# Optimization experiments

Measured on AMD Instinct MI355X. Metric: run time of the kernel, lower is better.

The kernel has to match this reference:

```python
import jax, jax.numpy as jnp
import numpy as np

N_HEAD = 16
HEAD_DIM = 32          # n_embed // n_head // 2
LAMBDA_INIT = 0.2      # 0.8 - 0.6*exp(-0.3*(layer-1)) with layer=1
ROPE_BASE = 10000.0
EPS = 1e-5


def _rope(x):
    # torchtune RotaryPositionalEmbeddings: interleaved adjacent pairs
    B, T, H, D = x.shape
    half = D // 2
    theta = ROPE_BASE ** (-(jnp.arange(half, dtype=jnp.float32) * 2.0 / D))  # [half]
    ang = jnp.arange(T, dtype=jnp.float32)[:, None] * theta[None, :]         # [T, half]
    cos = jnp.cos(ang)[None, :, None, :]
    sin = jnp.sin(ang)[None, :, None, :]
    xr = x.reshape(B, T, H, half, 2)
    x1, x2 = xr[..., 0], xr[..., 1]
    out = jnp.stack([x1 * cos - x2 * sin, x1 * sin + x2 * cos], axis=-1)
    return out.reshape(B, T, H, D).astype(x.dtype)


def reference(x, W_attn, W_proj, lambda_q1, lambda_k1, lambda_q2, lambda_k2):
    B, T, C = x.shape
    H, D = N_HEAD, HEAD_DIM
    qkv = x @ W_attn                              # [B,T,3C]
    q, k, v = jnp.split(qkv, 3, axis=-1)
    q = _rope(q.reshape(B, T, 2 * H, D)).transpose(0, 2, 1, 3)   # [B,2H,T,D]
    k = _rope(k.reshape(B, T, 2 * H, D)).transpose(0, 2, 1, 3)   # [B,2H,T,D]
    v = v.reshape(B, T, H, 2 * D).transpose(0, 2, 1, 3)          # [B,H,T,2D]

    lam = (jnp.exp(jnp.dot(lambda_q1, lambda_k1))
           - jnp.exp(jnp.dot(lambda_q2, lambda_k2)) + LAMBDA_INIT)

    # causal SDPA over both score paths (2H heads) in one pass, shared V
    scale = 1.0 / jnp.sqrt(jnp.asarray(D, x.dtype))
    scores = jnp.einsum('bhqd,bhkd->bhqk', q, k) * scale         # [B,2H,T,T]
    causal = jnp.tril(jnp.ones((T, T), dtype=bool))
    scores = jnp.where(causal, scores, jnp.finfo(scores.dtype).min)
    probs = jax.nn.softmax(scores, axis=-1)
    vv = jnp.concatenate([v, v], axis=1)                         # [B,2H,T,2D]
    A = jnp.einsum('bhqk,bhkd->bhqd', probs, vv)                 # [B,2H,T,2D]
    A1, A2 = A[:, :H], A[:, H:]

    diff = A1 - lam * A2                                         # [B,H,T,2D]
    # RMSNorm over last dim (2*head_dim), no affine, eps=1e-5
    diff = diff * jax.lax.rsqrt(jnp.mean(diff * diff, axis=-1, keepdims=True) + EPS)
    diff = (1.0 - LAMBDA_INIT) * diff
    out = diff.transpose(0, 2, 1, 3).reshape(B, T, C)
    return out @ W_proj


def setup_inputs() -> dict:
    key = jax.random.key(0)
    ks = jax.random.split(key, 7)
    B, T, C, D = 2, 2048, 1024, HEAD_DIM
    return {
        'x': jax.random.normal(ks[0], (B, T, C), jnp.float32),
        'W_attn': jax.random.normal(ks[1], (C, 3 * C), jnp.float32) * 0.02,
        'W_proj': jax.random.normal(ks[2], (C, C), jnp.float32) * 0.02,
        'lambda_q1': jax.random.normal(ks[3], (D,), jnp.float32) * 0.1,
        'lambda_k1': jax.random.normal(ks[4], (D,), jnp.float32) * 0.1,
        'lambda_q2': jax.random.normal(ks[5], (D,), jnp.float32) * 0.1,
        'lambda_k2': jax.random.normal(ks[6], (D,), jnp.float32) * 0.1,
    }
```

## Files before the change

### kernel.cpp

```cpp
#include <hip/hip_runtime.h>


typedef unsigned short u16;
typedef __bf16 bf16x8 __attribute__((ext_vector_type(8)));
typedef float f32x4 __attribute__((ext_vector_type(4)));
typedef float f32x16 __attribute__((ext_vector_type(16)));
typedef unsigned u32x2 __attribute__((ext_vector_type(2)));

__device__ __forceinline__ u16 f2bf(float f) {
  return __builtin_bit_cast(u16, (__bf16)f);
}
__device__ __forceinline__ float bf2f(u16 u) {
  return (float)__builtin_bit_cast(__bf16, u);
}
__device__ __forceinline__ unsigned pk2(float a, float b) {
  return (unsigned)f2bf(a) | ((unsigned)f2bf(b) << 16);
}

__device__ __forceinline__ void gload16(const u16* g, u16* l) {
  __builtin_amdgcn_global_load_lds(
      (const __attribute__((address_space(1))) unsigned int*)g,
      (__attribute__((address_space(3))) unsigned int*)l, 16, 0, 0);
}

__device__ __forceinline__ void trans_body(const float* __restrict__ in,
                                           u16* __restrict__ out, int R, int Cn,
                                           int bx, int by, float (*tile)[33],
                                           int tx, int ty) {
  const int c0 = bx * 32, r0 = by * 32;
#pragma unroll
  for (int rr = 0; rr < 4; ++rr)
    tile[ty + rr * 8][tx] = in[(size_t)(r0 + ty + rr * 8) * Cn + c0 + tx];
  __syncthreads();
#pragma unroll
  for (int rr = 0; rr < 4; ++rr)
    out[(size_t)(c0 + ty + rr * 8) * R + r0 + tx] = f2bf(tile[tx][ty + rr * 8]);
}

__global__ __launch_bounds__(256) void prep_kernel(
    const float* __restrict__ x, const float* __restrict__ Wa,
    const float* __restrict__ Wp, const float* __restrict__ lq1,
    const float* __restrict__ lk1, const float* __restrict__ lq2,
    const float* __restrict__ lk2, u16* __restrict__ xb, u16* __restrict__ WaT,
    u16* __restrict__ WpT, float2* __restrict__ Tab, float* __restrict__ lamp) {
  __shared__ float tile[32][33];
  const int id = blockIdx.x;
  const int tx = threadIdx.x & 31, ty = threadIdx.x >> 5;
  if (id < 4096) {
    const int i = id * 256 + threadIdx.x;
    float4 v = ((const float4*)x)[i];
    ushort4 o;
    o.x = f2bf(v.x); o.y = f2bf(v.y); o.z = f2bf(v.z); o.w = f2bf(v.w);
    ((ushort4*)xb)[i] = o;
  } else if (id < 7168) {
    const int t = id - 4096;
    trans_body(Wa, WaT, 1024, 3072, t % 96, t / 96, tile, tx, ty);
  } else if (id < 8192) {
    const int t = id - 7168;
    trans_body(Wp, WpT, 1024, 1024, t & 31, t >> 5, tile, tx, ty);
  } else if (id < 8320) {
    const int idx = (id - 8192) * 256 + threadIdx.x;
    const int t = idx >> 4, i = idx & 15;
    const float theta = exp2f(-0.83048202372184059f * (float)i);
    float sn, cs;
    sincosf((float)t * theta, &sn, &cs);
    Tab[idx] = make_float2(cs, sn);
  } else if (threadIdx.x == 0) {
    float d1 = 0.f, d2 = 0.f;
#pragma unroll
    for (int i = 0; i < 32; ++i) {
      d1 += lq1[i] * lk1[i];
      d2 += lq2[i] * lk2[i];
    }
    *lamp = expf(d1) - expf(d2) + 0.2f;
  }
}

__global__ __launch_bounds__(256) void gemm_qkv_kernel(
    const u16* __restrict__ A, const u16* __restrict__ BT,
    u16* __restrict__ Q, u16* __restrict__ K, u16* __restrict__ VT,
    const float2* __restrict__ Tab) {
  const int Kdim = 1024;
  __shared__ u16 As[128 * 32];
  __shared__ u16 Bs[128 * 32];
  const int tid = threadIdx.x;
  const int l = tid & 63;
  const int w = tid >> 6;
  const int nwgx = gridDim.x;
  const int lin = blockIdx.x + nwgx * blockIdx.y;
  const int cpx = (nwgx * gridDim.y) >> 3;
  const int swz = (lin & 7) * cpx + (lin >> 3);
  const int bm = swz / nwgx, bn = swz % nwgx;
  const int wm = w >> 1, wn = w & 1;
  const int rowA0 = bm * 128, rowB0 = bn * 128;
  const int r_ = tid >> 2;
  const int s_ = (tid & 3) * 8;
  const u16* Ag = &A[(size_t)(rowA0 + r_) * Kdim + s_];
  const u16* Bg = &BT[(size_t)(rowB0 + r_) * Kdim + s_];
  const size_t rstride = (size_t)64 * Kdim;
  f32x4 acc[4][4] = {};
  for (int k0 = 0; k0 < Kdim; k0 += 32) {
    gload16(Ag + k0, &As[r_ * 32 + s_]);
    gload16(Ag + rstride + k0, &As[2048 + r_ * 32 + s_]);
    gload16(Bg + k0, &Bs[r_ * 32 + s_]);
    gload16(Bg + rstride + k0, &Bs[2048 + r_ * 32 + s_]);
    __syncthreads();
    bf16x8 a[4], b[4];
#pragma unroll
    for (int i = 0; i < 4; ++i)
      a[i] = *(const bf16x8*)&As[(wm * 64 + i * 16 + (l & 15)) * 32 + (l >> 4) * 8];
#pragma unroll
    for (int j = 0; j < 4; ++j)
      b[j] = *(const bf16x8*)&Bs[(wn * 64 + j * 16 + (l & 15)) * 32 + (l >> 4) * 8];
#pragma unroll
    for (int i = 0; i < 4; ++i)
#pragma unroll
      for (int j = 0; j < 4; ++j)
        acc[i][j] = __builtin_amdgcn_mfma_f32_16x16x32_bf16(a[i], b[j], acc[i][j], 0, 0, 0);
    __syncthreads();
  }
  const int cr = (l >> 4) * 4;
  const int cc = l & 15;
  const int region = bn >> 3;
  if (region < 2) {
    const float qsc_ = (region == 0) ? 0.25503486f : 1.0f;
    u16* dst = (region == 0) ? Q : K;
#pragma unroll
    for (int i = 0; i < 4; ++i) {
      const int row0 = rowA0 + wm * 64 + i * 16 + cr;
      const int b_ = row0 >> 11, t0 = row0 & 2047;
#pragma unroll
      for (int j = 0; j < 4; ++j) {
        const int c = (bn & 7) * 128 + wn * 64 + j * 16 + cc;
        const int hh = c >> 5, d = c & 31;
        const int ii = d >> 1;
        const float sgn = (d & 1) ? 1.0f : -1.0f;
        const size_t base = (size_t)(b_ * 32 + hh) * 2048;
#pragma unroll
        for (int r = 0; r < 4; ++r) {
          const int t = t0 + r;
          const float2 cs = Tab[t * 16 + ii];
          const float xv = acc[i][j][r];
          const float px = __shfl_xor(xv, 1, 64);
          dst[(base + t) * 32 + d] = f2bf((xv * cs.x + sgn * px * cs.y) * qsc_);
        }
      }
    }
  } else {
#pragma unroll
    for (int i = 0; i < 4; ++i) {
      const int row0 = rowA0 + wm * 64 + i * 16 + cr;
      const int b_ = row0 >> 11, t0 = row0 & 2047;
#pragma unroll
      for (int j = 0; j < 4; ++j) {
        const int c3 = (bn & 7) * 128 + wn * 64 + j * 16 + cc;
        const int hv = c3 >> 6, dv = c3 & 63;
        ushort4 ov;
        ov.x = f2bf(acc[i][j][0]);
        ov.y = f2bf(acc[i][j][1]);
        ov.z = f2bf(acc[i][j][2]);
        ov.w = f2bf(acc[i][j][3]);
        *(ushort4*)&VT[((size_t)(b_ * 16 + hv) * 64 + dv) * 2048 + t0] = ov;
      }
    }
  }
}

__global__ __launch_bounds__(256) void gemm_out_kernel(
    const u16* __restrict__ A, const u16* __restrict__ BT, float* __restrict__ Cout,
    int Mdim, int Ndim, int Kdim) {
  __shared__ u16 As[64 * 32];
  __shared__ u16 Bs[128 * 32];
  const int tid = threadIdx.x;
  const int l = tid & 63;
  const int w = tid >> 6;
  const int nwgx = gridDim.x;
  const int lin = blockIdx.x + nwgx * blockIdx.y;
  const int cpx = (nwgx * gridDim.y) >> 3;
  const int swz = (lin & 7) * cpx + (lin >> 3);
  const int bm = swz / nwgx, bn = swz % nwgx;
  const int wm = w >> 1, wn = w & 1;
  const int rowA0 = bm * 64, rowB0 = bn * 128;
  const int r_ = tid >> 2;
  const int s_ = (tid & 3) * 8;
  const u16* Ag = &A[(size_t)(rowA0 + r_) * Kdim + s_];
  const u16* Bg = &BT[(size_t)(rowB0 + r_) * Kdim + s_];
  const size_t rstride = (size_t)64 * Kdim;
  f32x4 acc[2][4] = {};
  for (int k0 = 0; k0 < Kdim; k0 += 32) {
    gload16(Ag + k0, &As[r_ * 32 + s_]);
    gload16(Bg + k0, &Bs[r_ * 32 + s_]);
    gload16(Bg + rstride + k0, &Bs[2048 + r_ * 32 + s_]);
    __syncthreads();
    bf16x8 a[2], b[4];
#pragma unroll
    for (int i = 0; i < 2; ++i)
      a[i] = *(const bf16x8*)&As[(wm * 32 + i * 16 + (l & 15)) * 32 + (l >> 4) * 8];
#pragma unroll
    for (int j = 0; j < 4; ++j)
      b[j] = *(const bf16x8*)&Bs[(wn * 64 + j * 16 + (l & 15)) * 32 + (l >> 4) * 8];
#pragma unroll
    for (int i = 0; i < 2; ++i)
#pragma unroll
      for (int j = 0; j < 4; ++j)
        acc[i][j] = __builtin_amdgcn_mfma_f32_16x16x32_bf16(a[i], b[j], acc[i][j], 0, 0, 0);
    __syncthreads();
  }
  const int cr = (l >> 4) * 4;
  const int cc = l & 15;
#pragma unroll
  for (int i = 0; i < 2; ++i)
#pragma unroll
    for (int j = 0; j < 4; ++j)
#pragma unroll
      for (int r = 0; r < 4; ++r) {
        const int row = rowA0 + wm * 32 + i * 16 + cr + r;
        const int col = rowB0 + wn * 64 + j * 16 + cc;
        Cout[(size_t)row * Ndim + col] = acc[i][j][r];
      }
}

__global__ __launch_bounds__(256, 4) void attn_kernel(const u16* __restrict__ Q,
                                                      const u16* __restrict__ K,
                                                      const u16* __restrict__ VT,
                                                      u16* __restrict__ PO0,
                                                      u16* __restrict__ PO1,
                                                      float* __restrict__ ML) {
  __shared__ u16 Ks[64 * 34];
  __shared__ u16 Vs[64 * 66];
  __shared__ u16 Os[4 * 32 * 66];
  const int tid = threadIdx.x, l = tid & 63, w = tid >> 6;
  const int pp = blockIdx.x & 7, hf = blockIdx.x >> 3;
  const int h = blockIdx.y, b = blockIdx.z;
  const size_t qkbase = (size_t)(b * 32 + h) * 2048;
  const size_t vtb = (size_t)(b * 16 + (h & 15)) * 64;
  const int lq = l & 31, hi = l >> 5;
  const f32x16 z16 = {};
  const int krow = tid >> 2, ksl = (tid & 3) * 8;
  const int dva = tid >> 3, vsl = (tid & 7) * 8;
  const int dvb = dva + 32;
  const __bf16 one1 = (__bf16)1.0f;
  const bf16x8 ones = {one1, one1, one1, one1, one1, one1, one1, one1};

  for (int halfidx = 0; halfidx < 2; ++halfidx) {
    const int qt = halfidx ? (15 - pp) : pp;
    const int slot = hf ^ halfidx;
    const int s_begin = slot ? (qt + 1) : 0;
    const int s_end = slot ? (2 * qt + 2) : (qt + 1);
    const int q0 = qt * 128;
    const int qw = q0 + w * 32;
    const int q = qw + lq;
    const bf16x8 qf0 = *(const bf16x8*)&Q[(qkbase + q) * 32 + hi * 8];
    const bf16x8 qf1 = *(const bf16x8*)&Q[(qkbase + q) * 32 + 16 + hi * 8];
    f32x16 olo = {}, ohi = {}, lacc = {};
    const u16* pK = &K[(qkbase + s_begin * 64 + krow) * 32 + ksl];
    const u16* pV0 = &VT[(vtb + dva) * 2048 + s_begin * 64 + vsl];
    const u16* pV1 = &VT[(vtb + dvb) * 2048 + s_begin * 64 + vsl];
    uint4 kreg = *(const uint4*)pK;
    uint4 vreg0 = *(const uint4*)pV0;
    uint4 vreg1 = *(const uint4*)pV1;
    for (int s = s_begin; s < s_end; ++s) {
      const int kb = s * 64;
      *(uint4*)&Ks[krow * 34 + ksl] = kreg;
      *(uint4*)&Vs[dva * 66 + vsl] = vreg0;
      *(uint4*)&Vs[dvb * 66 + vsl] = vreg1;
      const int adv = (s + 1 < s_end) ? 1 : 0;
      pK += adv * 2048;
      pV0 += adv * 64;
      pV1 += adv * 64;
      kreg = *(const uint4*)pK;
      vreg0 = *(const uint4*)pV0;
      vreg1 = *(const uint4*)pV1;
      __syncthreads();
      if (qw + 31 >= kb) {
        f32x16 s0_, s1_;
        {
          const bf16x8 ka0 = *(const bf16x8*)&Ks[lq * 34 + hi * 8];
          const bf16x8 ka1 = *(const bf16x8*)&Ks[lq * 34 + 16 + hi * 8];
          const bf16x8 kc0 = *(const bf16x8*)&Ks[(32 + lq) * 34 + hi * 8];
          const bf16x8 kc1 = *(const bf16x8*)&Ks[(32 + lq) * 34 + 16 + hi * 8];
          __builtin_amdgcn_s_setprio(1);
          s0_ = __builtin_amdgcn_mfma_f32_32x32x16_bf16(ka0, qf0, z16, 0, 0, 0);
          s0_ = __builtin_amdgcn_mfma_f32_32x32x16_bf16(ka1, qf1, s0_, 0, 0, 0);
          s1_ = __builtin_amdgcn_mfma_f32_32x32x16_bf16(kc0, qf0, z16, 0, 0, 0);
          s1_ = __builtin_amdgcn_mfma_f32_32x32x16_bf16(kc1, qf1, s1_, 0, 0, 0);
          __builtin_amdgcn_s_setprio(0);
        }
        const bool nm = (kb + 63 > qw);
        if (nm) {
#pragma unroll
          for (int r = 0; r < 16; ++r) {
            const int kr = (r & 3) + 8 * (r >> 2) + 4 * hi;
            if (kb + kr > q) s0_[r] = -1e30f;
            if (kb + 32 + kr > q) s1_[r] = -1e30f;
          }
        }
#pragma unroll
        for (int r = 0; r < 16; ++r) {
          s0_[r] = __builtin_amdgcn_exp2f(s0_[r]);
          s1_[r] = __builtin_amdgcn_exp2f(s1_[r]);
        }
        unsigned pw[16];
#pragma unroll
        for (int j = 0; j < 8; ++j) {
          pw[j] = pk2(s0_[2 * j], s0_[2 * j + 1]);
          pw[8 + j] = pk2(s1_[2 * j], s1_[2 * j + 1]);
        }
        bf16x8 pa[4];
#pragma unroll
        for (int fidx = 0; fidx < 4; ++fidx) {
          const unsigned* wt = &pw[fidx * 4];
          union { unsigned u[4]; bf16x8 v; } fr;
#if __has_builtin(__builtin_amdgcn_permlane32_swap)
          const u32x2 rA = __builtin_amdgcn_permlane32_swap(wt[0], wt[2], false, false);
          const u32x2 rB = __builtin_amdgcn_permlane32_swap(wt[1], wt[3], false, false);
          fr.u[0] = rA[0]; fr.u[1] = rB[0]; fr.u[2] = rA[1]; fr.u[3] = rB[1];
#else
          const unsigned ua = hi ? wt[0] : wt[2];
          const unsigned ub = hi ? wt[1] : wt[3];
          const unsigned sa = __shfl_xor(ua, 32, 64);
          const unsigned sb = __shfl_xor(ub, 32, 64);
          fr.u[0] = hi ? sa : wt[0];
          fr.u[1] = hi ? sb : wt[1];
          fr.u[2] = hi ? wt[2] : sa;
          fr.u[3] = hi ? wt[3] : sb;
#endif
          pa[fidx] = fr.v;
        }
        __builtin_amdgcn_s_setprio(1);
#pragma unroll
        for (int ks = 0; ks < 4; ++ks) {
          const bf16x8 va = *(const bf16x8*)&Vs[lq * 66 + ks * 16 + hi * 8];
          const bf16x8 vb = *(const bf16x8*)&Vs[(32 + lq) * 66 + ks * 16 + hi * 8];
          olo = __builtin_amdgcn_mfma_f32_32x32x16_bf16(va, pa[ks], olo, 0, 0, 0);
          ohi = __builtin_amdgcn_mfma_f32_32x32x16_bf16(vb, pa[ks], ohi, 0, 0, 0);
          lacc = __builtin_amdgcn_mfma_f32_32x32x16_bf16(ones, pa[ks], lacc, 0, 0, 0);
        }
        __builtin_amdgcn_s_setprio(0);
      }
      __syncthreads();
    }
    const float lsum = lacc[0];
    const float inv = (lsum > 0.f) ? (1.0f / lsum) : 0.f;
    if (hi == 0)
      ML[(size_t)slot * 131072 + qkbase + q] = lsum;
    u16* Ow = &Os[(w * 32 + lq) * 66];
#pragma unroll
    for (int g = 0; g < 4; ++g) {
      const int d0 = 8 * g + 4 * hi;
      *(unsigned*)&Ow[d0] = pk2(olo[4 * g] * inv, olo[4 * g + 1] * inv);
      *(unsigned*)&Ow[d0 + 2] = pk2(olo[4 * g + 2] * inv, olo[4 * g + 3] * inv);
      *(unsigned*)&Ow[32 + d0] = pk2(ohi[4 * g] * inv, ohi[4 * g + 1] * inv);
      *(unsigned*)&Ow[32 + d0 + 2] = pk2(ohi[4 * g + 2] * inv, ohi[4 * g + 3] * inv);
    }
    __syncthreads();
    u16* PO = slot ? PO1 : PO0;
    for (int s2 = tid; s2 < 1024; s2 += 256) {
      const int wv = s2 >> 8, qq = (s2 >> 3) & 31, sl = (s2 & 7) * 8;
      *(uint4*)&PO[(qkbase + q0 + wv * 32 + qq) * 64 + sl] =
          *(const uint4*)&Os[(wv * 32 + qq) * 66 + sl];
    }
    __syncthreads();
  }
}

__global__ __launch_bounds__(256) void diff_rms_kernel(
    const u16* __restrict__ PO0, const u16* __restrict__ PO1,
    const float* __restrict__ ML, const float* __restrict__ lamp,
    u16* __restrict__ Mb) {
  const int g = threadIdx.x >> 5;
  const int dl = (threadIdx.x & 31) * 2;
  const int ridx = blockIdx.x * 8 + g;
  const int b = ridx >> 15, rem = ridx & 32767, h = rem >> 11, t = rem & 2047;
  const float lam = *lamp;
  const size_t row1 = (size_t)(b * 32 + h) * 2048 + t;
  const size_t row2 = (size_t)(b * 32 + 16 + h) * 2048 + t;
  const float lA1 = ML[row1], lB1 = ML[131072 + row1];
  const float lA2 = ML[row2], lB2 = ML[131072 + row2];
  const float i1 = 1.0f / (lA1 + lB1);
  const float wa1 = lA1 * i1, wb1 = lB1 * i1;
  const float i2 = 1.0f / (lA2 + lB2);
  const float wa2 = lA2 * i2, wb2 = lB2 * i2;
  const ushort2 p01 = *(const ushort2*)&PO0[row1 * 64 + dl];
  const ushort2 p11 = *(const ushort2*)&PO1[row1 * 64 + dl];
  const ushort2 p02 = *(const ushort2*)&PO0[row2 * 64 + dl];
  const ushort2 p12 = *(const ushort2*)&PO1[row2 * 64 + dl];
  const float a1x = wa1 * bf2f(p01.x) + wb1 * bf2f(p11.x);
  const float a1y = wa1 * bf2f(p01.y) + wb1 * bf2f(p11.y);
  const float a2x = wa2 * bf2f(p02.x) + wb2 * bf2f(p12.x);
  const float a2y = wa2 * bf2f(p02.y) + wb2 * bf2f(p12.y);
  const float df0 = a1x - lam * a2x;
  const float df1 = a1y - lam * a2y;
  float ss = df0 * df0 + df1 * df1;
  ss += __shfl_xor(ss, 1, 64);
  ss += __shfl_xor(ss, 2, 64);
  ss += __shfl_xor(ss, 4, 64);
  ss += __shfl_xor(ss, 8, 64);
  ss += __shfl_xor(ss, 16, 64);
  const float rms = rsqrtf(ss * (1.0f / 64.0f) + 1e-5f);
  ushort2 o;
  o.x = f2bf(0.8f * df0 * rms);
  o.y = f2bf(0.8f * df1 * rms);
  *(ushort2*)&Mb[((size_t)(b * 2048 + t)) * 1024 + h * 64 + dl] = o;
}

extern "C" void kernel_launch(void* const* d_in, const int* in_sizes, int n_in,
                              void* d_out, int out_size, void* d_ws, size_t ws_size,
                              hipStream_t stream) {
  const float* x = (const float*)d_in[0];
  const float* Wa = (const float*)d_in[1];
  const float* Wp = (const float*)d_in[2];
  const float* lq1 = (const float*)d_in[3];
  const float* lk1 = (const float*)d_in[4];
  const float* lq2 = (const float*)d_in[5];
  const float* lk2 = (const float*)d_in[6];
  if (ws_size < (size_t)(64u << 20)) return;

  char* ws = (char*)d_ws;
  u16* Qarr = (u16*)(ws);
  u16* Karr = (u16*)(ws + (8u << 20));
  u16* VTarr = (u16*)(ws + (16u << 20));
  u16* WpT = (u16*)(ws + (24u << 20));
  char* arena = ws + (26u << 20);
  u16* xb = (u16*)(arena);
  u16* WaT = (u16*)(arena + (8u << 20));
  float2* Tab = (float2*)(arena + (14u << 20));
  u16* PO0 = (u16*)(arena);
  u16* PO1 = (u16*)(arena + (16u << 20));
  float* ML = (float*)(arena + (32u << 20));
  float* lamp = (float*)(arena + (33u << 20));
  u16* Mbuf = Qarr;

  prep_kernel<<<8321, 256, 0, stream>>>(x, Wa, Wp, lq1, lk1, lq2, lk2,
                                        xb, WaT, WpT, Tab, lamp);
  gemm_qkv_kernel<<<dim3(24, 32), 256, 0, stream>>>(xb, WaT, Qarr, Karr, VTarr, Tab);
  attn_kernel<<<dim3(16, 32, 2), 256, 0, stream>>>(Qarr, Karr, VTarr, PO0, PO1, ML);
  diff_rms_kernel<<<8192, 256, 0, stream>>>(PO0, PO1, ML, lamp, Mbuf);
  gemm_out_kernel<<<dim3(8, 64), 256, 0, stream>>>(Mbuf, WpT, (float*)d_out, 4096, 1024, 1024);
}
```

Measured before the change: 142.6 us.

## Stage QKV GEMM epilogue through LDS for coalesced 16-byte stores

The QKV GEMM epilogue now writes RoPE'd Q/K tiles and the transposed V tile into shared memory first, then issues coalesced 16-byte global stores, instead of scattered 2-byte and 8-byte stores straight from the MFMA accumulator layout. Shared memory is merged into a single 32KB buffer so it can be reused for the staging. The V path is staged in two halves with extra barriers. The attention loop also recomputes K/V prefetch addresses from the tile index instead of advancing pointers, which is mostly a cosmetic or register-pressure change.

```diff
diff --git a/kernel.cpp b/kernel.cpp
--- a/kernel.cpp
+++ b/kernel.cpp
@@ -81,8 +81,9 @@
     u16* __restrict__ Q, u16* __restrict__ K, u16* __restrict__ VT,
     const float2* __restrict__ Tab) {
   const int Kdim = 1024;
-  __shared__ u16 As[128 * 32];
-  __shared__ u16 Bs[128 * 32];
+  __shared__ u16 SH[16384];
+  u16* As = SH;
+  u16* Bs = SH + 8192;
   const int tid = threadIdx.x;
   const int l = tid & 63;
   const int w = tid >> 6;
@@ -122,46 +123,68 @@
   const int cr = (l >> 4) * 4;
   const int cc = l & 15;
   const int region = bn >> 3;
+  const int b_ = rowA0 >> 11, tb = rowA0 & 2047;
   if (region < 2) {
     const float qsc_ = (region == 0) ? 0.25503486f : 1.0f;
     u16* dst = (region == 0) ? Q : K;
 #pragma unroll
     for (int i = 0; i < 4; ++i) {
-      const int row0 = rowA0 + wm * 64 + i * 16 + cr;
-      const int b_ = row0 >> 11, t0 = row0 & 2047;
+      const int trow0 = wm * 64 + i * 16 + cr;
 #pragma unroll
       for (int j = 0; j < 4; ++j) {
-        const int c = (bn & 7) * 128 + wn * 64 + j * 16 + cc;
-        const int hh = c >> 5, d = c & 31;
+        const int cL = wn * 64 + j * 16 + cc;
+        const int d = cL & 31;
         const int ii = d >> 1;
         const float sgn = (d & 1) ? 1.0f : -1.0f;
-        const size_t base = (size_t)(b_ * 32 + hh) * 2048;
 #pragma unroll
         for (int r = 0; r < 4; ++r) {
-          const int t = t0 + r;
+          const int t = tb + trow0 + r;
           const float2 cs = Tab[t * 16 + ii];
           const float xv = acc[i][j][r];
           const float px = __shfl_xor(xv, 1, 64);
-          dst[(base + t) * 32 + d] = f2bf((xv * cs.x + sgn * px * cs.y) * qsc_);
+          SH[(trow0 + r) * 128 + cL] = f2bf((xv * cs.x + sgn * px * cs.y) * qsc_);
         }
       }
     }
+    __syncthreads();
+#pragma unroll
+    for (int p = 0; p < 8; ++p) {
+      const int idx = p * 256 + tid;
+      const int trow = idx >> 4;
+      const int c8 = (idx & 15) * 8;
+      const int cG = (bn & 7) * 128 + c8;
+      const int hh = cG >> 5, d = cG & 31;
+      *(uint4*)&dst[((size_t)(b_ * 32 + hh) * 2048 + tb + trow) * 32 + d] =
+          *(const uint4*)&SH[trow * 128 + c8];
+    }
   } else {
 #pragma unroll
-    for (int i = 0; i < 4; ++i) {
-      const int row0 = rowA0 + wm * 64 + i * 16 + cr;
-      const int b_ = row0 >> 11, t0 = row0 & 2047;
-#pragma unroll
-      for (int j = 0; j < 4; ++j) {
-        const int c3 = (bn & 7) * 128 + wn * 64 + j * 16 + cc;
-        const int hv = c3 >> 6, dv = c3 & 63;
-        ushort4 ov;
-        ov.x = f2bf(acc[i][j][0]);
-        ov.y = f2bf(acc[i][j][1]);
-        ov.z = f2bf(acc[i][j][2]);
-        ov.w = f2bf(acc[i][j][3]);
-        *(ushort4*)&VT[((size_t)(b_ * 16 + hv) * 64 + dv) * 2048 + t0] = ov;
+    for (int th = 0; th < 2; ++th) {
+      if (wm == th) {
+#pragma unroll
+        for (int i = 0; i < 4; ++i) {
+          const int tr0 = i * 16 + cr;
+#pragma unroll
+          for (int j = 0; j < 4; ++j) {
+            const int cL = wn * 64 + j * 16 + cc;
+#pragma unroll
+            for (int r = 0; r < 4; ++r)
+              SH[cL * 66 + tr0 + r] = f2bf(acc[i][j][r]);
+          }
+        }
       }
+      __syncthreads();
+#pragma unroll
+      for (int p = 0; p < 4; ++p) {
+        const int idx = p * 256 + tid;
+        const int c = idx >> 3;
+        const int t8 = (idx & 7) * 8;
+        const int cG = (bn & 7) * 128 + c;
+        const int hv = cG >> 6, dv = cG & 63;
+        *(uint4*)&VT[((size_t)(b_ * 16 + hv) * 64 + dv) * 2048 + tb + th * 64 + t8] =
+            *(const uint4*)&SH[c * 66 + t8];
+      }
+      __syncthreads();
     }
   }
 }
@@ -253,24 +276,18 @@
     const bf16x8 qf0 = *(const bf16x8*)&Q[(qkbase + q) * 32 + hi * 8];
     const bf16x8 qf1 = *(const bf16x8*)&Q[(qkbase + q) * 32 + 16 + hi * 8];
     f32x16 olo = {}, ohi = {}, lacc = {};
-    const u16* pK = &K[(qkbase + s_begin * 64 + krow) * 32 + ksl];
-    const u16* pV0 = &VT[(vtb + dva) * 2048 + s_begin * 64 + vsl];
-    const u16* pV1 = &VT[(vtb + dvb) * 2048 + s_begin * 64 + vsl];
-    uint4 kreg = *(const uint4*)pK;
-    uint4 vreg0 = *(const uint4*)pV0;
-    uint4 vreg1 = *(const uint4*)pV1;
+    uint4 kreg = *(const uint4*)&K[(qkbase + s_begin * 64 + krow) * 32 + ksl];
+    uint4 vreg0 = *(const uint4*)&VT[(vtb + dva) * 2048 + s_begin * 64 + vsl];
+    uint4 vreg1 = *(const uint4*)&VT[(vtb + dvb) * 2048 + s_begin * 64 + vsl];
     for (int s = s_begin; s < s_end; ++s) {
       const int kb = s * 64;
       *(uint4*)&Ks[krow * 34 + ksl] = kreg;
       *(uint4*)&Vs[dva * 66 + vsl] = vreg0;
       *(uint4*)&Vs[dvb * 66 + vsl] = vreg1;
-      const int adv = (s + 1 < s_end) ? 1 : 0;
-      pK += adv * 2048;
-      pV0 += adv * 64;
-      pV1 += adv * 64;
-      kreg = *(const uint4*)pK;
-      vreg0 = *(const uint4*)pV0;
-      vreg1 = *(const uint4*)pV1;
+      const int sn = (s + 1 < s_end) ? (s + 1) : s;
+      kreg = *(const uint4*)&K[(qkbase + sn * 64 + krow) * 32 + ksl];
+      vreg0 = *(const uint4*)&VT[(vtb + dva) * 2048 + sn * 64 + vsl];
+      vreg1 = *(const uint4*)&VT[(vtb + dvb) * 2048 + sn * 64 + vsl];
       __syncthreads();
       if (qw + 31 >= kb) {
         f32x16 s0_, s1_;
```

New measurement: 141.0 us. About the same (-1.1%).
